# Optimization experiments

Measured on AMD Instinct MI355X. Metric: run time of the kernel, lower is better.

The kernel has to match this reference:

```python
import jax, jax.numpy as jnp
import numpy as np

B, S, D, H, E, K = 4, 2048, 1024, 2048, 8, 2


def setup_inputs() -> dict:
    key = jax.random.key(0)
    ks = jax.random.split(key, 6)
    s_d = 1.0 / np.sqrt(D)
    s_h = 1.0 / np.sqrt(H)
    return {
        "x": jax.random.normal(ks[0], (B, S, D), dtype=jnp.float32),
        "Wg": jax.random.normal(ks[1], (D, E), dtype=jnp.float32) * s_d,
        "bg": jnp.zeros((E,), dtype=jnp.float32),
        "w1": jax.random.normal(ks[2], (E, D, H), dtype=jnp.float32) * s_d,
        "w3": jax.random.normal(ks[3], (E, D, H), dtype=jnp.float32) * s_d,
        "w2": jax.random.normal(ks[4], (E, H, D), dtype=jnp.float32) * s_h,
    }


def reference(x, Wg, bg, w1, w3, w2):
    # Router (eval mode: no noise). logits: [B,S,E]
    logits = jnp.einsum("bsd,de->bse", x, Wg) + bg
    top_v, top_i = jax.lax.top_k(logits, K)          # [B,S,K]
    probs = jax.nn.softmax(top_v, axis=-1)           # softmax over -inf-masked logits == softmax over top-k
    # Scatter top-k probs back to dense gates [B,S,E] (zeros elsewhere)
    gates = jnp.sum(jax.nn.one_hot(top_i, E, dtype=x.dtype) * probs[..., None], axis=-2)
    # Combine: gate-weighted sum of per-expert SwiGLU FFN outputs.
    # gates[...,e] == 0 exactly for tokens not routed to expert e, matching the
    # original masked gather -> FFN -> weighted scatter-add.
    out = jnp.zeros_like(x)
    for e in range(E):
        h = jax.nn.silu(x @ w1[e]) * (x @ w3[e])     # [B,S,H]
        y = h @ w2[e]                                # [B,S,D]
        out = out + gates[..., e:e + 1] * y
    return out
```

## Files before the change

kernel.cpp:

```cpp
#include <hip/hip_runtime.h>

typedef short bf16x8 __attribute__((ext_vector_type(8)));
typedef float f32x4 __attribute__((ext_vector_type(4)));
typedef unsigned short u16;
typedef unsigned int u32;

#define TOKS 8192
#define DDIM 1024
#define HDIM 2048
#define NEXP 8
#define ROWS_TOTAL (2 * TOKS)

#define WL1_CAP 544
#define WL2_CAP 136

#define NSUB 32
#define SUBCAP 256
#define CSTRIDE 32

__device__ __forceinline__ u16 f2b(float f) {
  u32 x;
  __builtin_memcpy(&x, &f, 4);
  return (u16)((x + 0x7fffu + ((x >> 16) & 1u)) >> 16);
}

typedef const __attribute__((address_space(1))) u32* gp_t;
typedef __attribute__((address_space(3))) u32* lp_t;
__device__ __forceinline__ void glds16(const void* g, void* l) {
  __builtin_amdgcn_global_load_lds((gp_t)g, (lp_t)l, 16, 0, 0);
}

__global__ __launch_bounds__(256) void cvt_wT_kernel(const float* __restrict__ in,
                                                     u16* __restrict__ out, int K, int N) {
  size_t eo = (size_t)blockIdx.z * K * N;
  in += eo; out += eo;
  int n0 = blockIdx.x * 64, k0 = blockIdx.y * 64;
  __shared__ u16 s[64][72];
  int tid = threadIdx.x;
  int kr = tid >> 4, nc = (tid & 15) * 4;
#pragma unroll
  for (int i = 0; i < 4; ++i) {
    int k = k0 + i * 16 + kr;
    float4 v = *(const float4*)(in + (size_t)k * N + n0 + nc);
    ushort4 u;
    u.x = f2b(v.x); u.y = f2b(v.y); u.z = f2b(v.z); u.w = f2b(v.w);
    *(ushort4*)&s[i * 16 + kr][nc] = u;
  }
  __syncthreads();
  int nl = tid >> 2, kc = tid & 3;
  union { int4 v[2]; u16 u[16]; } o;
#pragma unroll
  for (int j = 0; j < 16; ++j) o.u[j] = s[kc * 16 + j][nl];
  u16* op = out + (size_t)(n0 + nl) * K + k0 + kc * 16;
  *(int4*)op = o.v[0];
  *(int4*)(op + 8) = o.v[1];
}

__global__ __launch_bounds__(256) void cvt_wc_kernel(const float* __restrict__ w1,
                                                     const float* __restrict__ w3,
                                                     u16* __restrict__ out, int K, int N) {
  int z = blockIdx.z;
  int e = z >> 1, half = z & 1;
  const float* in = (half ? w3 : w1) + (size_t)e * K * N;
  out += (size_t)e * 2 * K * N;
  int n0 = blockIdx.x * 64, k0 = blockIdx.y * 64;
  __shared__ u16 s[64][72];
  int tid = threadIdx.x;
  int kr = tid >> 4, nc = (tid & 15) * 4;
#pragma unroll
  for (int i = 0; i < 4; ++i) {
    int k = k0 + i * 16 + kr;
    float4 v = *(const float4*)(in + (size_t)k * N + n0 + nc);
    ushort4 u;
    u.x = f2b(v.x); u.y = f2b(v.y); u.z = f2b(v.z); u.w = f2b(v.w);
    *(ushort4*)&s[i * 16 + kr][nc] = u;
  }
  __syncthreads();
  int nl = tid >> 2, kc = tid & 3;
  union { int4 v[2]; u16 u[16]; } o;
#pragma unroll
  for (int j = 0; j < 16; ++j) o.u[j] = s[kc * 16 + j][nl];
  int n = n0 + nl;
  int orow = ((n >> 4) << 5) + half * 16 + (n & 15);
  u16* op = out + (size_t)orow * K + k0 + kc * 16;
  *(int4*)op = o.v[0];
  *(int4*)(op + 8) = o.v[1];
}

__global__ __launch_bounds__(256) void router_kernel(
    const float* __restrict__ x, const float* __restrict__ Wg,
    const float* __restrict__ bg, int* __restrict__ counts32,
    int* __restrict__ tok16, float* __restrict__ g16, u16* __restrict__ xb) {
  int lane = threadIdx.x & 63;
  int t = blockIdx.x * 4 + (threadIdx.x >> 6);
  int sub = blockIdx.x & (NSUB - 1);
  const float* xr = x + (size_t)t * DDIM;
  u16* xo = xb + (size_t)t * DDIM;
  float acc[NEXP];
#pragma unroll
  for (int e = 0; e < NEXP; ++e) acc[e] = 0.f;
#pragma unroll
  for (int jj = 0; jj < DDIM / 256; ++jj) {
    int d = jj * 256 + lane * 4;
    float4 xv = *(const float4*)(xr + d);
    ushort4 o;
    o.x = f2b(xv.x); o.y = f2b(xv.y); o.z = f2b(xv.z); o.w = f2b(xv.w);
    *(ushort4*)(xo + d) = o;
    float xs[4] = {xv.x, xv.y, xv.z, xv.w};
#pragma unroll
    for (int dd = 0; dd < 4; ++dd) {
      float4 w0 = *(const float4*)(Wg + (d + dd) * NEXP);
      float4 w1v = *(const float4*)(Wg + (d + dd) * NEXP + 4);
      acc[0] += xs[dd] * w0.x; acc[1] += xs[dd] * w0.y;
      acc[2] += xs[dd] * w0.z; acc[3] += xs[dd] * w0.w;
      acc[4] += xs[dd] * w1v.x; acc[5] += xs[dd] * w1v.y;
      acc[6] += xs[dd] * w1v.z; acc[7] += xs[dd] * w1v.w;
    }
  }
#pragma unroll
  for (int off = 32; off > 0; off >>= 1) {
#pragma unroll
    for (int e = 0; e < NEXP; ++e) acc[e] += __shfl_down(acc[e], off, 64);
  }
  if (lane == 0) {
    float v[NEXP];
#pragma unroll
    for (int e = 0; e < NEXP; ++e) v[e] = acc[e] + bg[e];
    int e0 = 0;
    float v0 = v[0];
#pragma unroll
    for (int e = 1; e < NEXP; ++e)
      if (v[e] > v0) { v0 = v[e]; e0 = e; }
    int e1 = -1;
    float v1 = -3.4e38f;
#pragma unroll
    for (int e = 0; e < NEXP; ++e)
      if (e != e0 && v[e] > v1) { v1 = v[e]; e1 = e; }
    if (e1 < 0) e1 = (e0 + 1) & 7;
    float ex = __expf(v1 - v0);
    float g0 = 1.f / (1.f + ex);
    float g1 = 1.f - g0;
    int c0 = sub * NEXP + e0;
    int s0 = atomicAdd(&counts32[c0 * CSTRIDE], 1);
    if (s0 < SUBCAP) { tok16[c0 * SUBCAP + s0] = t; g16[c0 * SUBCAP + s0] = g0; }
    int c1 = sub * NEXP + e1;
    int s1 = atomicAdd(&counts32[c1 * CSTRIDE], 1);
    if (s1 < SUBCAP) { tok16[c1 * SUBCAP + s1] = t; g16[c1 * SUBCAP + s1] = g1; }
  }
}

__global__ void offsets_kernel(const int* __restrict__ counts32, int* __restrict__ counts,
                               int* __restrict__ offsets, int* __restrict__ dstbase,
                               int* __restrict__ wl1, int* __restrict__ wl2) {
  int t = threadIdx.x;
  __shared__ int sc[NEXP];
  if (t < NEXP) {
    int c[NSUB];
#pragma unroll
    for (int sub = 0; sub < NSUB; ++sub) c[sub] = counts32[(sub * NEXP + t) * CSTRIDE];
    int run = 0;
#pragma unroll
    for (int sub = 0; sub < NSUB; ++sub) { dstbase[sub * NEXP + t] = run; run += c[sub]; }
    counts[t] = run;
    sc[t] = run;
  }
  __syncthreads();
  if (t == 0) {
    int o = 0;
    for (int e = 0; e < NEXP; ++e) { offsets[e] = o; o += sc[e]; }
    int j1 = 0, j2 = 0;
    for (int e = 0; e < NEXP; ++e) {
      int me = (sc[e] + 127) >> 7;
      for (int m = 0; m < me; ++m) {
        if (j1 + 4 <= WL1_CAP) {
#pragma unroll
          for (int yq = 0; yq < 4; ++yq) wl1[1 + j1 + yq] = (e << 8) | (m << 2) | yq;
          j1 += 4;
        }
        if (j2 < WL2_CAP) wl2[1 + j2++] = (e << 8) | m;
      }
    }
    wl1[0] = j1; wl2[0] = j2;
  }
}

__global__ __launch_bounds__(256) void compact_kernel(
    const int* __restrict__ counts32, const int* __restrict__ dstbase,
    const int* __restrict__ offsets,
    const int* __restrict__ tok16, const float* __restrict__ g16,
    int* __restrict__ tok_ids, float* __restrict__ gates,
    int* __restrict__ posc, int* __restrict__ pos) {
  int idx = blockIdx.x;
  int e = idx & (NEXP - 1);
  int n = counts32[idx * CSTRIDE];
  if (n > SUBCAP) n = SUBCAP;
  int base = dstbase[idx];
  int eoff = offsets[e];
  for (int i = threadIdx.x; i < n; i += 256) {
    int t = tok16[idx * SUBCAP + i];
    tok_ids[e * TOKS + base + i] = t;
    gates[e * TOKS + base + i]   = g16[idx * SUBCAP + i];
    int slot = atomicAdd(&posc[t], 1);
    if (slot < 2) pos[t * 2 + slot] = eoff + base + i;
  }
}

__global__ __launch_bounds__(256) void combine_kernel(
    const float* __restrict__ y2, const int* __restrict__ pos,
    float* __restrict__ out) {
  int t = blockIdx.x;
  int r0 = pos[2 * t], r1 = pos[2 * t + 1];
  int c = threadIdx.x * 4;
  float4 a = *(const float4*)(y2 + (size_t)r0 * DDIM + c);
  float4 b = *(const float4*)(y2 + (size_t)r1 * DDIM + c);
  float4 o;
  o.x = a.x + b.x; o.y = a.y + b.y; o.z = a.z + b.z; o.w = a.w + b.w;
  *(float4*)(out + (size_t)t * DDIM + c) = o;
}

__global__ __launch_bounds__(256, 4) void ffn1_kernel(
    const u16* __restrict__ xb, const u16* __restrict__ wc,
    const int* __restrict__ tok_ids, const int* __restrict__ counts,
    const int* __restrict__ offsets, const int* __restrict__ wl,
    u16* __restrict__ h, int nbase_wc, int hw, int e_arg) {
  int e, m, y;
  if (e_arg >= 0) {
    e = e_arg; m = blockIdx.x; y = blockIdx.y;
    if (m * 128 >= counts[e]) return;
  } else {
    int bid = blockIdx.x;
    int xcd = bid & 7, j = bid >> 3;
    if (j >= wl[0]) return;
    int w = wl[1 + j];
    e = w >> 8; m = (w >> 2) & 63; y = xcd * 4 + (w & 3);
  }
  int count = counts[e];
  int mbase = m * 128;
  int row_off = (e_arg >= 0) ? 0 : offsets[e];
  int n0w = nbase_wc + y * 128;
  size_t we = (e_arg >= 0) ? 0 : (size_t)e;
  const u16* wce = wc + we * (size_t)(2 * HDIM * DDIM);

  __shared__ u16 sA[128 * 64];
  __shared__ u16 sB[128 * 64];
  __shared__ int stok[128];

  int tid = threadIdx.x, lane = tid & 63, wv = tid >> 6;
  if (tid < 128) {
    int s = mbase + tid;
    if (s >= count) s = count - 1;
    stok[tid] = tok_ids[e * TOKS + s];
  }
  __syncthreads();

  int rloc = lane >> 3, ch = lane & 7;
  u32 offA[4], offB[4];
#pragma unroll
  for (int i = 0; i < 4; ++i) {
    int r = (wv * 4 + i) * 8 + rloc;
    int sw = ch ^ (r & 7);
    offA[i] = (u32)stok[r] * DDIM + sw * 8;
    offB[i] = (u32)(n0w + r) * DDIM + sw * 8;
  }

  int wm = wv >> 1, wn = wv & 1;
  int rsel = lane & 15, q = lane >> 4;

  f32x4 acc[4][4];
#pragma unroll
  for (int i = 0; i < 4; ++i)
#pragma unroll
    for (int j = 0; j < 4; ++j) {
      f32x4 z = {0.f, 0.f, 0.f, 0.f};
      acc[i][j] = z;
    }

  for (int k0 = 0; k0 < DDIM; k0 += 64) {
    __syncthreads();
#pragma unroll
    for (int i = 0; i < 4; ++i) {
      int sbase = (wv * 4 + i) * 512;
      glds16(xb  + offA[i] + k0, sA + sbase);
      glds16(wce + offB[i] + k0, sB + sbase);
    }
    __syncthreads();

#pragma unroll
    for (int ks = 0; ks < 2; ++ks) {
      bf16x8 aF[4], bF[4];
#pragma unroll
      for (int mi = 0; mi < 4; ++mi) {
        int r = wm * 64 + mi * 16 + rsel;
        int p = (ks * 4 + q) ^ (r & 7);
        aF[mi] = *(const bf16x8*)&sA[r * 64 + p * 8];
      }
#pragma unroll
      for (int ni = 0; ni < 4; ++ni) {
        int r = wn * 64 + ni * 16 + rsel;
        int p = (ks * 4 + q) ^ (r & 7);
        bF[ni] = *(const bf16x8*)&sB[r * 64 + p * 8];
      }
#pragma unroll
      for (int mi = 0; mi < 4; ++mi)
#pragma unroll
        for (int ni = 0; ni < 4; ++ni)
          acc[mi][ni] = __builtin_amdgcn_mfma_f32_16x16x32_bf16(aF[mi], bF[ni], acc[mi][ni], 0, 0, 0);
    }
  }

  int cm = count - mbase;
#pragma unroll
  for (int mi = 0; mi < 4; ++mi) {
#pragma unroll
    for (int rr = 0; rr < 4; ++rr) {
      int mrow = wm * 64 + mi * 16 + q * 4 + rr;
      if (mrow < cm) {
#pragma unroll
        for (int np = 0; np < 2; ++np) {
          int hcol = y * 64 + (wn * 2 + np) * 16 + rsel;
          float u = acc[mi][2 * np][rr];
          float vv = acc[mi][2 * np + 1][rr];
          float hv = (u / (1.f + __expf(-u))) * vv;
          h[(size_t)(row_off + mbase + mrow) * hw + hcol] = f2b(hv);
        }
      }
    }
  }
}

__global__ __launch_bounds__(256) void ffn2_kernel(
    const u16* __restrict__ h, const u16* __restrict__ w2t,
    const int* __restrict__ tok_ids, const float* __restrict__ gates,
    const int* __restrict__ counts, const int* __restrict__ offsets,
    const int* __restrict__ wl, float* __restrict__ out,
    float* __restrict__ y2, int kbase, int hw, int e_arg) {
  int e, m, y;
  if (e_arg >= 0) {
    e = e_arg; m = blockIdx.x; y = blockIdx.y;
    if (m * 128 >= counts[e]) return;
  } else {
    int bid = blockIdx.x;
    int xcd = bid & 7, j = bid >> 3;
    if (j >= wl[0]) return;
    int w = wl[1 + j];
    e = w >> 8; m = w & 63; y = xcd;
  }
  int count = counts[e];
  int mbase = m * 128;
  int row_off = (e_arg >= 0) ? 0 : offsets[e];
  int n0 = y * 128;
  size_t we = (e_arg >= 0) ? 0 : (size_t)e;
  const u16* w2e = w2t + we * (size_t)(HDIM * DDIM);

  __shared__ u16 sA[128 * 64];
  __shared__ u16 sB[128 * 64];
  __shared__ int stok[128];
  __shared__ float sg[128];

  int tid = threadIdx.x, lane = tid & 63, wv = tid >> 6;
  if (tid < 128) {
    int s = mbase + tid;
    if (s >= count) s = count - 1;
    stok[tid] = tok_ids[e * TOKS + s];
    sg[tid] = gates[e * TOKS + s];
  }
  __syncthreads();

  int rloc = lane >> 3, ch = lane & 7;
  u32 offA[4], offB[4];
#pragma unroll
  for (int i = 0; i < 4; ++i) {
    int r = (wv * 4 + i) * 8 + rloc;
    int sw = ch ^ (r & 7);
    int slot = mbase + r;
    if (slot >= count) slot = count - 1;
    offA[i] = (u32)(row_off + slot) * hw + sw * 8;
    offB[i] = (u32)(n0 + r) * HDIM + kbase + sw * 8;
  }

  int wm = wv >> 1, wn = wv & 1;
  int rsel = lane & 15, q = lane >> 4;

  f32x4 acc[4][4];
#pragma unroll
  for (int i = 0; i < 4; ++i)
#pragma unroll
    for (int j = 0; j < 4; ++j) {
      f32x4 z = {0.f, 0.f, 0.f, 0.f};
      acc[i][j] = z;
    }

  for (int k0 = 0; k0 < hw; k0 += 64) {
    __syncthreads();
#pragma unroll
    for (int i = 0; i < 4; ++i) {
      int sbase = (wv * 4 + i) * 512;
      glds16(h   + offA[i] + k0, sA + sbase);
      glds16(w2e + offB[i] + k0, sB + sbase);
    }
    __syncthreads();

#pragma unroll
    for (int ks = 0; ks < 2; ++ks) {
      bf16x8 aF[4], bF[4];
#pragma unroll
      for (int mi = 0; mi < 4; ++mi) {
        int r = wm * 64 + mi * 16 + rsel;
        int p = (ks * 4 + q) ^ (r & 7);
        aF[mi] = *(const bf16x8*)&sA[r * 64 + p * 8];
      }
#pragma unroll
      for (int ni = 0; ni < 4; ++ni) {
        int r = wn * 64 + ni * 16 + rsel;
        int p = (ks * 4 + q) ^ (r & 7);
        bF[ni] = *(const bf16x8*)&sB[r * 64 + p * 8];
      }
#pragma unroll
      for (int mi = 0; mi < 4; ++mi)
#pragma unroll
        for (int ni = 0; ni < 4; ++ni)
          acc[mi][ni] = __builtin_amdgcn_mfma_f32_16x16x32_bf16(aF[mi], bF[ni], acc[mi][ni], 0, 0, 0);
    }
  }

  int cm = count - mbase;
#pragma unroll
  for (int mi = 0; mi < 4; ++mi) {
#pragma unroll
    for (int rr = 0; rr < 4; ++rr) {
      int mrow = wm * 64 + mi * 16 + q * 4 + rr;
      if (mrow < cm) {
        float g = sg[mrow];
        if (y2) {
          size_t rbase = (size_t)(row_off + mbase + mrow) * DDIM;
#pragma unroll
          for (int ni = 0; ni < 4; ++ni) {
            int col = n0 + wn * 64 + ni * 16 + rsel;
            y2[rbase + col] = g * acc[mi][ni][rr];
          }
        } else {
          int t = stok[mrow];
#pragma unroll
          for (int ni = 0; ni < 4; ++ni) {
            int col = n0 + wn * 64 + ni * 16 + rsel;
            atomicAdd(&out[(size_t)t * DDIM + col], g * acc[mi][ni][rr]);
          }
        }
      }
    }
  }
}

extern "C" void kernel_launch(void* const* d_in, const int* in_sizes, int n_in,
                              void* d_out, int out_size, void* d_ws, size_t ws_size,
                              hipStream_t stream) {
  (void)in_sizes; (void)n_in; (void)out_size;
  const float* x  = (const float*)d_in[0];
  const float* Wg = (const float*)d_in[1];
  const float* bg = (const float*)d_in[2];
  const float* w1 = (const float*)d_in[3];
  const float* w3 = (const float*)d_in[4];
  const float* w2 = (const float*)d_in[5];
  float* out = (float*)d_out;

  char* ws = (char*)d_ws;
  int*   tok_ids  = (int*)ws;
  float* gates    = (float*)(ws + 262144);
  int*   counts   = (int*)(ws + 524288);
  int*   offsets  = (int*)(ws + 524352);
  int*   wl1      = (int*)(ws + 524416);
  int*   wl2      = (int*)(ws + 528512);
  int*   dstbase  = (int*)(ws + 529536);
  int*   counts32 = (int*)(ws + 532480);
  int*   posc     = (int*)(ws + 565248);
  int*   tok16    = (int*)(ws + 598016);
  float* g16      = (float*)(ws + 860160);
  int*   pos      = (int*)(ws + 1122304);
  u16*   xb       = (u16*)(ws + (2 << 20));

  const size_t WEXP  = (size_t)HDIM * DDIM * 2;
  const size_t WALL  = 3ull * NEXP * WEXP;
  const size_t HFULL = (size_t)ROWS_TOTAL * HDIM * 2;
  const size_t Y2SZ  = (size_t)ROWS_TOTAL * DDIM * 4;
  const size_t base  = (2 << 20) + 16777216ull;

  hipMemsetAsync(counts32, 0, 65536, stream);

  router_kernel<<<TOKS / 4, 256, 0, stream>>>(x, Wg, bg, counts32, tok16, g16, xb);
  offsets_kernel<<<1, 64, 0, stream>>>(counts32, counts, offsets, dstbase, wl1, wl2);
  compact_kernel<<<NSUB * NEXP, 256, 0, stream>>>(counts32, dstbase, offsets, tok16, g16,
                                                  tok_ids, gates, posc, pos);

  if (ws_size >= base + WALL + HFULL + Y2SZ) {
    u16* wcb = (u16*)(ws + base);
    u16* w2t = wcb + (size_t)NEXP * 2 * HDIM * DDIM;
    u16* hb  = w2t + (size_t)NEXP * HDIM * DDIM;
    float* y2 = (float*)(hb + (size_t)ROWS_TOTAL * HDIM);
    cvt_wc_kernel<<<dim3(HDIM / 64, DDIM / 64, 2 * NEXP), 256, 0, stream>>>(
        w1, w3, wcb, DDIM, HDIM);
    cvt_wT_kernel<<<dim3(DDIM / 64, HDIM / 64, NEXP), 256, 0, stream>>>(w2, w2t, HDIM, DDIM);
    ffn1_kernel<<<dim3(8 * WL1_CAP), 256, 0, stream>>>(
        xb, wcb, tok_ids, counts, offsets, wl1, hb, 0, HDIM, -1);
    ffn2_kernel<<<dim3(8 * WL2_CAP), 256, 0, stream>>>(
        hb, w2t, tok_ids, gates, counts, offsets, wl2, out, y2, 0, HDIM, -1);
    combine_kernel<<<TOKS, 256, 0, stream>>>(y2, pos, out);
  } else if (ws_size >= base + WALL + HFULL) {
    u16* wcb = (u16*)(ws + base);
    u16* w2t = wcb + (size_t)NEXP * 2 * HDIM * DDIM;
    u16* hb  = w2t + (size_t)NEXP * HDIM * DDIM;
    hipMemsetAsync(out, 0, (size_t)TOKS * DDIM * 4, stream);
    cvt_wc_kernel<<<dim3(HDIM / 64, DDIM / 64, 2 * NEXP), 256, 0, stream>>>(
        w1, w3, wcb, DDIM, HDIM);
    cvt_wT_kernel<<<dim3(DDIM / 64, HDIM / 64, NEXP), 256, 0, stream>>>(w2, w2t, HDIM, DDIM);
    ffn1_kernel<<<dim3(8 * WL1_CAP), 256, 0, stream>>>(
        xb, wcb, tok_ids, counts, offsets, wl1, hb, 0, HDIM, -1);
    ffn2_kernel<<<dim3(8 * WL2_CAP), 256, 0, stream>>>(
        hb, w2t, tok_ids, gates, counts, offsets, wl2, out, nullptr, 0, HDIM, -1);
  } else {
    int hw = 128;
    const int cand[5] = {2048, 1024, 512, 256, 128};
    for (int i = 0; i < 5; ++i)
      if (base + 3 * WEXP + (size_t)TOKS * cand[i] * 2 <= ws_size) { hw = cand[i]; break; }
    u16* wcb = (u16*)(ws + base);
    u16* w2t = wcb + (size_t)2 * HDIM * DDIM;
    u16* hb  = w2t + (size_t)HDIM * DDIM;
    hipMemsetAsync(out, 0, (size_t)TOKS * DDIM * 4, stream);
    for (int e = 0; e < NEXP; ++e) {
      cvt_wc_kernel<<<dim3(HDIM / 64, DDIM / 64, 2), 256, 0, stream>>>(
          w1 + (size_t)e * DDIM * HDIM, w3 + (size_t)e * DDIM * HDIM, wcb, DDIM, HDIM);
      cvt_wT_kernel<<<dim3(DDIM / 64, HDIM / 64, 1), 256, 0, stream>>>(
          w2 + (size_t)e * HDIM * DDIM, w2t, HDIM, DDIM);
      for (int nb = 0; nb < HDIM; nb += hw) {
        ffn1_kernel<<<dim3(64, hw / 64, 1), 256, 0, stream>>>(
            xb, wcb, tok_ids, counts, offsets, nullptr, hb, 2 * nb, hw, e);
        ffn2_kernel<<<dim3(64, DDIM / 128, 1), 256, 0, stream>>>(
            hb, w2t, tok_ids, gates, counts, offsets, nullptr, out, nullptr, nb, hw, e);
      }
    }
  }
}
```

Before: 552.5 us.

## Rewrite ffn1 as 256x256 tile, 512-thread kernel with double-buffered LDS pipeline

The first expert GEMM moves from 128x128 tiles and 256 threads to 256x256 tiles and 512 threads. Shared memory is split into two buffered quadrant stages, with global-to-LDS loads interleaved across eight MFMA phases using explicit vmcnt waits, barriers and setprio. The work list and grid indexing are updated to match the larger tiles. The aim is more reuse per tile and hiding load latency behind MFMA work, at the cost of more LDS, fewer blocks, and more padding waste on per-expert row counts.

```diff
diff --git a/kernel.cpp b/kernel.cpp
--- a/kernel.cpp
+++ b/kernel.cpp
@@ -11,7 +11,7 @@
 #define NEXP 8
 #define ROWS_TOTAL (2 * TOKS)
 
-#define WL1_CAP 544
+#define WL1_CAP 144
 #define WL2_CAP 136
 
 #define NSUB 32
@@ -170,15 +170,17 @@
     for (int e = 0; e < NEXP; ++e) { offsets[e] = o; o += sc[e]; }
     int j1 = 0, j2 = 0;
     for (int e = 0; e < NEXP; ++e) {
-      int me = (sc[e] + 127) >> 7;
-      for (int m = 0; m < me; ++m) {
-        if (j1 + 4 <= WL1_CAP) {
-#pragma unroll
-          for (int yq = 0; yq < 4; ++yq) wl1[1 + j1 + yq] = (e << 8) | (m << 2) | yq;
-          j1 += 4;
+      int me1 = (sc[e] + 255) >> 8;
+      for (int m = 0; m < me1; ++m) {
+        if (j1 + 2 <= WL1_CAP) {
+          wl1[1 + j1] = (e << 8) | (m << 1);
+          wl1[2 + j1] = (e << 8) | (m << 1) | 1;
+          j1 += 2;
         }
+      }
+      int me2 = (sc[e] + 127) >> 7;
+      for (int m = 0; m < me2; ++m)
         if (j2 < WL2_CAP) wl2[1 + j2++] = (e << 8) | m;
-      }
     }
     wl1[0] = j1; wl2[0] = j2;
   }
@@ -218,7 +220,7 @@
   *(float4*)(out + (size_t)t * DDIM + c) = o;
 }
 
-__global__ __launch_bounds__(256, 4) void ffn1_kernel(
+__global__ __launch_bounds__(512, 2) void ffn1_kernel(
     const u16* __restrict__ xb, const u16* __restrict__ wc,
     const int* __restrict__ tok_ids, const int* __restrict__ counts,
     const int* __restrict__ offsets, const int* __restrict__ wl,
@@ -226,27 +228,27 @@
   int e, m, y;
   if (e_arg >= 0) {
     e = e_arg; m = blockIdx.x; y = blockIdx.y;
-    if (m * 128 >= counts[e]) return;
+    if (m * 256 >= counts[e]) return;
   } else {
     int bid = blockIdx.x;
     int xcd = bid & 7, j = bid >> 3;
     if (j >= wl[0]) return;
     int w = wl[1 + j];
-    e = w >> 8; m = (w >> 2) & 63; y = xcd * 4 + (w & 3);
+    e = w >> 8; m = (w >> 1) & 63; y = xcd * 2 + (w & 1);
   }
   int count = counts[e];
-  int mbase = m * 128;
+  int mbase = m * 256;
   int row_off = (e_arg >= 0) ? 0 : offsets[e];
-  int n0w = nbase_wc + y * 128;
+  int n0w = nbase_wc + y * 256;
   size_t we = (e_arg >= 0) ? 0 : (size_t)e;
   const u16* wce = wc + we * (size_t)(2 * HDIM * DDIM);
 
-  __shared__ u16 sA[128 * 64];
-  __shared__ u16 sB[128 * 64];
-  __shared__ int stok[128];
+  __shared__ u16 sA[2][2][8192];
+  __shared__ u16 sB[2][2][8192];
+  __shared__ int stok[256];
 
   int tid = threadIdx.x, lane = tid & 63, wv = tid >> 6;
-  if (tid < 128) {
+  if (tid < 256) {
     int s = mbase + tid;
     if (s >= count) s = count - 1;
     stok[tid] = tok_ids[e * TOKS + s];
@@ -254,78 +256,112 @@
   __syncthreads();
 
   int rloc = lane >> 3, ch = lane & 7;
-  u32 offA[4], offB[4];
-#pragma unroll
-  for (int i = 0; i < 4; ++i) {
-    int r = (wv * 4 + i) * 8 + rloc;
-    int sw = ch ^ (r & 7);
-    offA[i] = (u32)stok[r] * DDIM + sw * 8;
-    offB[i] = (u32)(n0w + r) * DDIM + sw * 8;
-  }
-
-  int wm = wv >> 1, wn = wv & 1;
+  int swz8 = (ch ^ rloc) * 8;
+  u32 offA[2][2], offB[2][2];
+#pragma unroll
+  for (int hh = 0; hh < 2; ++hh)
+#pragma unroll
+    for (int s = 0; s < 2; ++s) {
+      int r = hh * 128 + s * 64 + wv * 8 + rloc;
+      offA[hh][s] = (u32)stok[r] * DDIM + swz8;
+      offB[hh][s] = (u32)(n0w + r) * DDIM + swz8;
+    }
+
+#define STAGE_A(c, hh, kt) do { \
+    glds16(xb + offA[hh][0] + (kt) * 64, &sA[c][hh][wv * 512]); \
+    glds16(xb + offA[hh][1] + (kt) * 64, &sA[c][hh][4096 + wv * 512]); } while (0)
+#define STAGE_B(c, hh, kt) do { \
+    glds16(wce + offB[hh][0] + (kt) * 64, &sB[c][hh][wv * 512]); \
+    glds16(wce + offB[hh][1] + (kt) * 64, &sB[c][hh][4096 + wv * 512]); } while (0)
+
+  int wm = wv >> 2, wn = wv & 3;
   int rsel = lane & 15, q = lane >> 4;
 
-  f32x4 acc[4][4];
-#pragma unroll
-  for (int i = 0; i < 4; ++i)
-#pragma unroll
-    for (int j = 0; j < 4; ++j) {
-      f32x4 z = {0.f, 0.f, 0.f, 0.f};
-      acc[i][j] = z;
-    }
-
-  for (int k0 = 0; k0 < DDIM; k0 += 64) {
-    __syncthreads();
-#pragma unroll
-    for (int i = 0; i < 4; ++i) {
-      int sbase = (wv * 4 + i) * 512;
-      glds16(xb  + offA[i] + k0, sA + sbase);
-      glds16(wce + offB[i] + k0, sB + sbase);
-    }
-    __syncthreads();
-
-#pragma unroll
-    for (int ks = 0; ks < 2; ++ks) {
-      bf16x8 aF[4], bF[4];
-#pragma unroll
-      for (int mi = 0; mi < 4; ++mi) {
-        int r = wm * 64 + mi * 16 + rsel;
-        int p = (ks * 4 + q) ^ (r & 7);
-        aF[mi] = *(const bf16x8*)&sA[r * 64 + p * 8];
-      }
-#pragma unroll
-      for (int ni = 0; ni < 4; ++ni) {
-        int r = wn * 64 + ni * 16 + rsel;
-        int p = (ks * 4 + q) ^ (r & 7);
-        bF[ni] = *(const bf16x8*)&sB[r * 64 + p * 8];
-      }
+  f32x4 acc[2][2][4][2];
+#pragma unroll
+  for (int a = 0; a < 2; ++a)
+#pragma unroll
+    for (int b = 0; b < 2; ++b)
 #pragma unroll
       for (int mi = 0; mi < 4; ++mi)
 #pragma unroll
-        for (int ni = 0; ni < 4; ++ni)
-          acc[mi][ni] = __builtin_amdgcn_mfma_f32_16x16x32_bf16(aF[mi], bF[ni], acc[mi][ni], 0, 0, 0);
-    }
-  }
+        for (int ni = 0; ni < 2; ++ni) {
+          f32x4 z = {0.f, 0.f, 0.f, 0.f};
+          acc[a][b][mi][ni] = z;
+        }
+
+#define PHASE(c, qa, qb, WAITS, ...) do { \
+    bf16x8 aF[4][2], bF[2][2]; \
+    _Pragma("unroll") for (int mi = 0; mi < 4; ++mi) { \
+      int rl = wm * 64 + mi * 16 + rsel; \
+      _Pragma("unroll") for (int ks = 0; ks < 2; ++ks) { \
+        int p = ((ks * 4 + q) ^ (rl & 7)) * 8; \
+        aF[mi][ks] = *(const bf16x8*)&sA[c][qa][rl * 64 + p]; \
+      } } \
+    _Pragma("unroll") for (int ni = 0; ni < 2; ++ni) { \
+      int rl = wn * 32 + ni * 16 + rsel; \
+      _Pragma("unroll") for (int ks = 0; ks < 2; ++ks) { \
+        int p = ((ks * 4 + q) ^ (rl & 7)) * 8; \
+        bF[ni][ks] = *(const bf16x8*)&sB[c][qb][rl * 64 + p]; \
+      } } \
+    __VA_ARGS__; \
+    WAITS; \
+    __builtin_amdgcn_s_barrier(); \
+    __builtin_amdgcn_s_setprio(1); \
+    _Pragma("unroll") for (int mi = 0; mi < 4; ++mi) \
+      _Pragma("unroll") for (int ni = 0; ni < 2; ++ni) \
+        _Pragma("unroll") for (int ks = 0; ks < 2; ++ks) \
+          acc[qa][qb][mi][ni] = __builtin_amdgcn_mfma_f32_16x16x32_bf16( \
+              aF[mi][ks], bF[ni][ks], acc[qa][qb][mi][ni], 0, 0, 0); \
+    __builtin_amdgcn_s_setprio(0); \
+    __builtin_amdgcn_s_barrier(); \
+  } while (0)
+
+  STAGE_A(0, 0, 0); STAGE_B(0, 0, 0); STAGE_A(0, 1, 0); STAGE_B(0, 1, 0);
+  STAGE_A(1, 0, 1); STAGE_B(1, 0, 1);
+  asm volatile("s_waitcnt vmcnt(4)" ::: "memory");
+  __builtin_amdgcn_s_barrier();
+
+  const int NI = DDIM / 128;
+  for (int i = 0; i < NI; ++i) {
+    int k1t = 2 * i + 1, k2t = 2 * i + 2, k3t = 2 * i + 3;
+    bool nl = (i + 1 < NI);
+    PHASE(0, 0, 0, , STAGE_A(1, 1, k1t));
+    PHASE(0, 0, 1, , STAGE_B(1, 1, k1t));
+    PHASE(0, 1, 0, , if (nl) STAGE_A(0, 0, k2t));
+    PHASE(0, 1, 1,
+          if (nl) asm volatile("s_waitcnt vmcnt(4)" ::: "memory");
+          else    asm volatile("s_waitcnt vmcnt(0)" ::: "memory"); ,
+          if (nl) STAGE_B(0, 0, k2t));
+    PHASE(1, 0, 0, , if (nl) STAGE_A(0, 1, k2t));
+    PHASE(1, 0, 1, , if (nl) STAGE_B(0, 1, k2t));
+    PHASE(1, 1, 0, , if (nl) STAGE_A(1, 0, k3t));
+    PHASE(1, 1, 1,
+          if (nl) asm volatile("s_waitcnt vmcnt(4)" ::: "memory"); ,
+          if (nl) STAGE_B(1, 0, k3t));
+  }
+#undef PHASE
+#undef STAGE_A
+#undef STAGE_B
 
   int cm = count - mbase;
 #pragma unroll
-  for (int mi = 0; mi < 4; ++mi) {
-#pragma unroll
-    for (int rr = 0; rr < 4; ++rr) {
-      int mrow = wm * 64 + mi * 16 + q * 4 + rr;
-      if (mrow < cm) {
-#pragma unroll
-        for (int np = 0; np < 2; ++np) {
-          int hcol = y * 64 + (wn * 2 + np) * 16 + rsel;
-          float u = acc[mi][2 * np][rr];
-          float vv = acc[mi][2 * np + 1][rr];
-          float hv = (u / (1.f + __expf(-u))) * vv;
-          h[(size_t)(row_off + mbase + mrow) * hw + hcol] = f2b(hv);
+  for (int a = 0; a < 2; ++a)
+#pragma unroll
+    for (int b = 0; b < 2; ++b)
+#pragma unroll
+      for (int mi = 0; mi < 4; ++mi)
+#pragma unroll
+        for (int rr = 0; rr < 4; ++rr) {
+          int mrow = a * 128 + wm * 64 + mi * 16 + q * 4 + rr;
+          if (mrow < cm) {
+            int hcol = y * 128 + b * 64 + wn * 16 + rsel;
+            float u = acc[a][b][mi][0][rr];
+            float vv = acc[a][b][mi][1][rr];
+            float hv = (u / (1.f + __expf(-u))) * vv;
+            h[(size_t)(row_off + mbase + mrow) * hw + hcol] = f2b(hv);
+          }
         }
-      }
-    }
-  }
 }
 
 __global__ __launch_bounds__(256) void ffn2_kernel(
@@ -499,7 +535,7 @@
     cvt_wc_kernel<<<dim3(HDIM / 64, DDIM / 64, 2 * NEXP), 256, 0, stream>>>(
         w1, w3, wcb, DDIM, HDIM);
     cvt_wT_kernel<<<dim3(DDIM / 64, HDIM / 64, NEXP), 256, 0, stream>>>(w2, w2t, HDIM, DDIM);
-    ffn1_kernel<<<dim3(8 * WL1_CAP), 256, 0, stream>>>(
+    ffn1_kernel<<<dim3(8 * WL1_CAP), 512, 0, stream>>>(
         xb, wcb, tok_ids, counts, offsets, wl1, hb, 0, HDIM, -1);
     ffn2_kernel<<<dim3(8 * WL2_CAP), 256, 0, stream>>>(
         hb, w2t, tok_ids, gates, counts, offsets, wl2, out, y2, 0, HDIM, -1);
@@ -512,7 +548,7 @@
     cvt_wc_kernel<<<dim3(HDIM / 64, DDIM / 64, 2 * NEXP), 256, 0, stream>>>(
         w1, w3, wcb, DDIM, HDIM);
     cvt_wT_kernel<<<dim3(DDIM / 64, HDIM / 64, NEXP), 256, 0, stream>>>(w2, w2t, HDIM, DDIM);
-    ffn1_kernel<<<dim3(8 * WL1_CAP), 256, 0, stream>>>(
+    ffn1_kernel<<<dim3(8 * WL1_CAP), 512, 0, stream>>>(
         xb, wcb, tok_ids, counts, offsets, wl1, hb, 0, HDIM, -1);
     ffn2_kernel<<<dim3(8 * WL2_CAP), 256, 0, stream>>>(
         hb, w2t, tok_ids, gates, counts, offsets, wl2, out, nullptr, 0, HDIM, -1);
@@ -531,7 +567,7 @@
       cvt_wT_kernel<<<dim3(DDIM / 64, HDIM / 64, 1), 256, 0, stream>>>(
           w2 + (size_t)e * HDIM * DDIM, w2t, HDIM, DDIM);
       for (int nb = 0; nb < HDIM; nb += hw) {
-        ffn1_kernel<<<dim3(64, hw / 64, 1), 256, 0, stream>>>(
+        ffn1_kernel<<<dim3(TOKS / 256, hw / 128, 1), 512, 0, stream>>>(
             xb, wcb, tok_ids, counts, offsets, nullptr, hb, 2 * nb, hw, e);
         ffn2_kernel<<<dim3(64, DDIM / 128, 1), 256, 0, stream>>>(
             hb, w2t, tok_ids, gates, counts, offsets, nullptr, out, nullptr, nb, hw, e);
```

Measured after the change: 611.5 us. 10.7% more time.
